# Performance work log

Hardware: AMD Instinct MI355X
Metric: run time of the kernel (lower is better)

The kernel has to match this reference:

```python
import jax, jax.numpy as jnp
import numpy as np
from jax import lax

RADIUS = 3
ITERATION = 6
KSIZE = 2 * RADIUS + 1


def _make_kernels(r):
    # Build the 8 directional side-window box kernels, order: L,R,U,D,NW,NE,SW,SE
    k = 2 * r + 1
    f = np.ones((k, k), np.float32)
    L = f.copy(); L[:, r + 1:] = 0
    R = f.copy(); R[:, :r] = 0
    U = f.copy(); U[r + 1:, :] = 0
    D = f.copy(); D[:r, :] = 0
    NW = U.copy(); NW[:, r + 1:] = 0
    NE = U.copy(); NE[:, :r] = 0
    SW = D.copy(); SW[:, r + 1:] = 0
    SE = D.copy(); SE[:, :r] = 0
    n_half = (r + 1) * k          # normalizer for half windows
    n_quarter = (r + 1) ** 2      # normalizer for quarter windows
    ks = np.stack([L / n_half, R / n_half, U / n_half, D / n_half,
                   NW / n_quarter, NE / n_quarter, SW / n_quarter, SE / n_quarter])
    return jnp.asarray(ks[:, None, :, :])  # (8,1,k,k) OIHW


def setup_inputs() -> dict:
    key = jax.random.key(0)
    k1, k2 = jax.random.split(key)
    im = jax.random.normal(k1, (4, 3, 512, 512), dtype=jnp.float32)
    pert = jax.random.normal(k2, (4, 3, 512, 512), dtype=jnp.float32)
    return {"im": im, "pert": pert}


def reference(im, pert):
    b, c, h, w = im.shape
    W = _make_kernels(RADIUS)

    def conv8(x):  # (N,1,h,w) -> (N,8,h,w), SAME padding of radius
        return lax.conv_general_dilated(
            x, W, window_strides=(1, 1),
            padding=[(RADIUS, RADIUS), (RADIUS, RADIUS)],
            dimension_numbers=("NCHW", "OIHW", "NCHW"))

    # channels are processed independently with identical kernels -> fold c into batch
    im_f = im.reshape(b * c, 1, h, w)
    pert_f = pert.reshape(b * c, 1, h, w)

    def step(carry, _):
        im_ch, pert_ch = carry
        z = jnp.concatenate([im_ch, pert_ch], axis=0)  # (2N,1,h,w)
        dz = conv8(z) - z                              # (2N,8,h,w), broadcast over dir
        d, dd = jnp.split(dz, 2, axis=0)
        idx = jnp.argmin(jnp.abs(d), axis=1, keepdims=True)    # (N,1,h,w)
        dm = jnp.take_along_axis(d, idx, axis=1)
        ddm = jnp.take_along_axis(dd, idx, axis=1)
        return (im_ch + dm, pert_ch + ddm), None

    (im_f, pert_f), _ = lax.scan(step, (im_f, pert_f), None, length=ITERATION)
    # torch code overwrites every channel of res with pert_ch -> result is filtered pert
    return pert_f.reshape(b, c, h, w)
```

## Files before the change

### kernel.cpp

```cpp
#include <hip/hip_runtime.h>

#define HH 512
#define WW 512
#define NIMG 12
#define RAD 3
#define TW 64
#define TH 16
#define LW (TW + 2*RAD)
#define LH (TH + 2*RAD)
#define RPW 4

typedef float v2 __attribute__((ext_vector_type(2)));

__global__ __launch_bounds__(256) void swf_step(
    const float* __restrict__ im_in, const float* __restrict__ pe_in,
    float* __restrict__ im_out, float* __restrict__ pe_out)
{
    __shared__ float sI[LH][LW];
    __shared__ float sP[LH][LW];

    const int tid = threadIdx.x;
    const int x0 = blockIdx.x * TW;
    const int y0 = blockIdx.y * TH;
    const size_t base = (size_t)blockIdx.z * (size_t)(HH * WW);
    const float* imb = im_in + base;
    const float* peb = pe_in + base;

    for (int i = tid; i < LH * LW; i += 256) {
        int r = i / LW;
        int c = i - r * LW;
        int gy = y0 - RAD + r;
        int gx = x0 - RAD + c;
        bool ok = ((unsigned)gy < (unsigned)HH) && ((unsigned)gx < (unsigned)WW);
        int gi = gy * WW + gx;
        sI[r][c] = ok ? imb[gi] : 0.0f;
        sP[r][c] = ok ? peb[gi] : 0.0f;
    }
    __syncthreads();

    const float w28 = 1.0f / 28.0f;
    const float w16 = 0.0625f;
    const v2 w28v = {w28, w28};
    const v2 w16v = {w16, w16};
    const int tx = tid & 63;
    const int wv = tid >> 6;
    const int r0 = wv * RPW;

    float wi[7][7];
    v2    hlr[7];
    float cc[7];

    #pragma unroll
    for (int m = 0; m < 7; ++m) {
        #pragma unroll
        for (int dx = 0; dx < 7; ++dx)
            wi[m][dx] = sI[r0 + m][tx + dx];
        float b0 = sP[r0 + m][tx],     b1 = sP[r0 + m][tx + 1],
              b2 = sP[r0 + m][tx + 2], b3 = sP[r0 + m][tx + 3],
              b4 = sP[r0 + m][tx + 4], b5 = sP[r0 + m][tx + 5],
              b6 = sP[r0 + m][tx + 6];
        hlr[m] = (v2){(b0 + b1) + (b2 + b3), (b3 + b4) + (b5 + b6)};
        cc[m] = b3;
    }

    #pragma unroll
    for (int jj = 0; jj < RPW; ++jj) {
        v2 aLR = {0.f, 0.f};
        v2 aUD = {0.f, 0.f};
        v2 aQN = {0.f, 0.f};
        v2 aQS = {0.f, 0.f};
        #pragma unroll
        for (int dy = 0; dy < 7; ++dy) {
            const int s = (jj + dy) % 7;
            #pragma unroll
            for (int dx = 0; dx < 4; ++dx)
                aLR = __builtin_elementwise_fma(
                    (v2){wi[s][dx], wi[s][dx + 3]}, w28v, aLR);
        }
        #pragma unroll
        for (int dy = 0; dy < 4; ++dy) {
            const int su = (jj + dy) % 7;
            const int sd = (jj + dy + 3) % 7;
            #pragma unroll
            for (int dx = 0; dx < 7; ++dx)
                aUD = __builtin_elementwise_fma(
                    (v2){wi[su][dx], wi[sd][dx]}, w28v, aUD);
            #pragma unroll
            for (int dx = 0; dx < 4; ++dx) {
                aQN = __builtin_elementwise_fma(
                    (v2){wi[su][dx], wi[su][dx + 3]}, w16v, aQN);
                aQS = __builtin_elementwise_fma(
                    (v2){wi[sd][dx], wi[sd][dx + 3]}, w16v, aQS);
            }
        }

        const float cI = wi[(jj + 3) % 7][3];
        const v2 cI2 = {cI, cI};
        const v2 d01 = aLR - cI2;
        const v2 d23 = aUD - cI2;
        const v2 d45 = aQN - cI2;
        const v2 d67 = aQS - cI2;
        float d[8] = {d01.x, d01.y, d23.x, d23.y, d45.x, d45.y, d67.x, d67.y};

        float e[8];
        const int p0 = (jj + 0) % 7, p1 = (jj + 1) % 7, p2 = (jj + 2) % 7,
                  p3 = (jj + 3) % 7, p4 = (jj + 4) % 7, p5 = (jj + 5) % 7,
                  p6 = (jj + 6) % 7;
        const float cP = cc[p3];
        {
            v2 qN = ((hlr[p0] + hlr[p1]) + (hlr[p2] + hlr[p3]));
            v2 qS = ((hlr[p3] + hlr[p4]) + (hlr[p5] + hlr[p6]));
            float cu = ((cc[p0] + cc[p1]) + (cc[p2] + cc[p3]));
            float cd = ((cc[p3] + cc[p4]) + (cc[p5] + cc[p6]));
            const v2 cP2 = {cP, cP};
            v2 eLR = (qN + qS - hlr[p3]) * w28v - cP2;
            v2 eQN = qN * w16v - cP2;
            v2 eQS = qS * w16v - cP2;
            e[0] = eLR.x;  e[1] = eLR.y;
            e[2] = (qN.x + qN.y - cu) * w28 - cP;
            e[3] = (qS.x + qS.y - cd) * w28 - cP;
            e[4] = eQN.x;  e[5] = eQN.y;
            e[6] = eQS.x;  e[7] = eQS.y;
        }

        float bestAbs = fabsf(d[0]);
        float bd = d[0];
        float be = e[0];
        #pragma unroll
        for (int j = 1; j < 8; ++j) {
            float a = fabsf(d[j]);
            bool take = a < bestAbs;
            bestAbs = take ? a : bestAbs;
            bd = take ? d[j] : bd;
            be = take ? e[j] : be;
        }

        const int gy = y0 + r0 + jj;
        const int gx = x0 + tx;
        const size_t gi = base + (size_t)gy * WW + gx;
        im_out[gi] = cI + bd;
        pe_out[gi] = cP + be;

        if (jj < RPW - 1) {
            const int m = r0 + jj + 7;
            const int slot = jj % 7;
            #pragma unroll
            for (int dx = 0; dx < 7; ++dx)
                wi[slot][dx] = sI[m][tx + dx];
            float b0 = sP[m][tx],     b1 = sP[m][tx + 1], b2 = sP[m][tx + 2],
                  b3 = sP[m][tx + 3], b4 = sP[m][tx + 4], b5 = sP[m][tx + 5],
                  b6 = sP[m][tx + 6];
            hlr[slot] = (v2){(b0 + b1) + (b2 + b3), (b3 + b4) + (b5 + b6)};
            cc[slot] = b3;
        }
    }
}

extern "C" void kernel_launch(void* const* d_in, const int* in_sizes, int n_in,
                              void* d_out, int out_size, void* d_ws, size_t ws_size,
                              hipStream_t stream) {
    const float* im0 = (const float*)d_in[0];
    const float* pe0 = (const float*)d_in[1];
    float* out = (float*)d_out;

    const size_t npix = (size_t)NIMG * HH * WW;
    float* imA = (float*)d_ws;
    float* imB = imA + npix;
    float* peA = imB + npix;
    float* peB = out;

    dim3 grid(WW / TW, HH / TH, NIMG);
    dim3 block(256);

    swf_step<<<grid, block, 0, stream>>>(im0, pe0, imA, peA);
    swf_step<<<grid, block, 0, stream>>>(imA, peA, imB, peB);
    swf_step<<<grid, block, 0, stream>>>(imB, peB, imA, peA);
    swf_step<<<grid, block, 0, stream>>>(imA, peA, imB, peB);
    swf_step<<<grid, block, 0, stream>>>(imB, peB, imA, peA);
    swf_step<<<grid, block, 0, stream>>>(imA, peA, imB, out);
}
```

Baseline: 235.9 us.

## Fuse two filter iterations per kernel via shared-memory halo recompute

Each launch now runs two side-window iterations: it loads a 12-pixel-halo tile, computes an intermediate 38x64 region into a second shared buffer (zeroing out-of-image pixels to mimic SAME padding), then computes the final 32x58 tile from it. This halves the number of launches and the global-memory round trips, at the cost of redundant halo computation and a narrower 58-column output tile. The intermediate image write is also skipped on the last launch, and the register window is stored as pre-paired vectors for packed FMAs.

```diff
diff --git a/kernel.cpp b/kernel.cpp
--- a/kernel.cpp
+++ b/kernel.cpp
@@ -4,103 +4,88 @@
 #define WW 512
 #define NIMG 12
 #define RAD 3
-#define TW 64
-#define TH 16
-#define LW (TW + 2*RAD)
-#define LH (TH + 2*RAD)
-#define RPW 4
+
+#define TW 58
+#define TH 32
+#define IW 64
+#define IH 38
+#define IW2 72
+#define SW 70
+#define SH 46
+#define GX ((WW + TW - 1) / TW)
 
 typedef float v2 __attribute__((ext_vector_type(2)));
 
-__global__ __launch_bounds__(256) void swf_step(
-    const float* __restrict__ im_in, const float* __restrict__ pe_in,
-    float* __restrict__ im_out, float* __restrict__ pe_out)
+template <int RPW, int LDW, class F>
+__device__ __forceinline__ void ring_pass(
+    const float* __restrict__ SI, const float* __restrict__ SP,
+    int r0, int tx, F emit)
 {
-    __shared__ float sI[LH][LW];
-    __shared__ float sP[LH][LW];
-
-    const int tid = threadIdx.x;
-    const int x0 = blockIdx.x * TW;
-    const int y0 = blockIdx.y * TH;
-    const size_t base = (size_t)blockIdx.z * (size_t)(HH * WW);
-    const float* imb = im_in + base;
-    const float* peb = pe_in + base;
-
-    for (int i = tid; i < LH * LW; i += 256) {
-        int r = i / LW;
-        int c = i - r * LW;
-        int gy = y0 - RAD + r;
-        int gx = x0 - RAD + c;
-        bool ok = ((unsigned)gy < (unsigned)HH) && ((unsigned)gx < (unsigned)WW);
-        int gi = gy * WW + gx;
-        sI[r][c] = ok ? imb[gi] : 0.0f;
-        sP[r][c] = ok ? peb[gi] : 0.0f;
-    }
-    __syncthreads();
-
     const float w28 = 1.0f / 28.0f;
     const float w16 = 0.0625f;
     const v2 w28v = {w28, w28};
     const v2 w16v = {w16, w16};
-    const int tx = tid & 63;
-    const int wv = tid >> 6;
-    const int r0 = wv * RPW;
-
-    float wi[7][7];
+
+    v2    pi[7][4];
     v2    hlr[7];
     float cc[7];
 
+    auto rowload = [&](int slot, int m) {
+        const float* rI = SI + m * LDW + tx;
+        float w0 = rI[0], w1 = rI[1], w2 = rI[2], w3 = rI[3],
+              w4 = rI[4], w5 = rI[5], w6 = rI[6];
+        pi[slot][0] = (v2){w0, w3};
+        pi[slot][1] = (v2){w1, w4};
+        pi[slot][2] = (v2){w2, w5};
+        pi[slot][3] = (v2){w3, w6};
+        const float* rP = SP + m * LDW + tx;
+        float b0 = rP[0], b1 = rP[1], b2 = rP[2], b3 = rP[3],
+              b4 = rP[4], b5 = rP[5], b6 = rP[6];
+        hlr[slot] = (v2){(b0 + b1) + (b2 + b3), (b3 + b4) + (b5 + b6)};
+        cc[slot] = b3;
+    };
+
     #pragma unroll
-    for (int m = 0; m < 7; ++m) {
-        #pragma unroll
-        for (int dx = 0; dx < 7; ++dx)
-            wi[m][dx] = sI[r0 + m][tx + dx];
-        float b0 = sP[r0 + m][tx],     b1 = sP[r0 + m][tx + 1],
-              b2 = sP[r0 + m][tx + 2], b3 = sP[r0 + m][tx + 3],
-              b4 = sP[r0 + m][tx + 4], b5 = sP[r0 + m][tx + 5],
-              b6 = sP[r0 + m][tx + 6];
-        hlr[m] = (v2){(b0 + b1) + (b2 + b3), (b3 + b4) + (b5 + b6)};
-        cc[m] = b3;
-    }
+    for (int m = 0; m < 7; ++m)
+        rowload(m, r0 + m);
 
     #pragma unroll
     for (int jj = 0; jj < RPW; ++jj) {
-        v2 aLR = {0.f, 0.f};
-        v2 aUD = {0.f, 0.f};
-        v2 aQN = {0.f, 0.f};
-        v2 aQS = {0.f, 0.f};
+        v2 aLR = {0.f, 0.f}, aQN = {0.f, 0.f}, aQS = {0.f, 0.f};
         #pragma unroll
         for (int dy = 0; dy < 7; ++dy) {
             const int s = (jj + dy) % 7;
             #pragma unroll
             for (int dx = 0; dx < 4; ++dx)
-                aLR = __builtin_elementwise_fma(
-                    (v2){wi[s][dx], wi[s][dx + 3]}, w28v, aLR);
-        }
+                aLR = __builtin_elementwise_fma(pi[s][dx], w28v, aLR);
+        }
+        float U = 0.f, Dd = 0.f;
         #pragma unroll
         for (int dy = 0; dy < 4; ++dy) {
             const int su = (jj + dy) % 7;
             const int sd = (jj + dy + 3) % 7;
-            #pragma unroll
-            for (int dx = 0; dx < 7; ++dx)
-                aUD = __builtin_elementwise_fma(
-                    (v2){wi[su][dx], wi[sd][dx]}, w28v, aUD);
+            U = fmaf(pi[su][0].x, w28, U);  U = fmaf(pi[su][1].x, w28, U);
+            U = fmaf(pi[su][2].x, w28, U);  U = fmaf(pi[su][3].x, w28, U);
+            U = fmaf(pi[su][1].y, w28, U);  U = fmaf(pi[su][2].y, w28, U);
+            U = fmaf(pi[su][3].y, w28, U);
+            Dd = fmaf(pi[sd][0].x, w28, Dd); Dd = fmaf(pi[sd][1].x, w28, Dd);
+            Dd = fmaf(pi[sd][2].x, w28, Dd); Dd = fmaf(pi[sd][3].x, w28, Dd);
+            Dd = fmaf(pi[sd][1].y, w28, Dd); Dd = fmaf(pi[sd][2].y, w28, Dd);
+            Dd = fmaf(pi[sd][3].y, w28, Dd);
             #pragma unroll
             for (int dx = 0; dx < 4; ++dx) {
-                aQN = __builtin_elementwise_fma(
-                    (v2){wi[su][dx], wi[su][dx + 3]}, w16v, aQN);
-                aQS = __builtin_elementwise_fma(
-                    (v2){wi[sd][dx], wi[sd][dx + 3]}, w16v, aQS);
+                aQN = __builtin_elementwise_fma(pi[su][dx], w16v, aQN);
+                aQS = __builtin_elementwise_fma(pi[sd][dx], w16v, aQS);
             }
         }
 
-        const float cI = wi[(jj + 3) % 7][3];
+        const float cI = pi[(jj + 3) % 7][3].x;
         const v2 cI2 = {cI, cI};
         const v2 d01 = aLR - cI2;
-        const v2 d23 = aUD - cI2;
+        const float d2 = U - cI, d3 = Dd - cI;
         const v2 d45 = aQN - cI2;
         const v2 d67 = aQS - cI2;
-        float d[8] = {d01.x, d01.y, d23.x, d23.y, d45.x, d45.y, d67.x, d67.y};
+        float d[8] = {d01.x, d01.y, d2, d3, d45.x, d45.y, d67.x, d67.y};
 
         float e[8];
         const int p0 = (jj + 0) % 7, p1 = (jj + 1) % 7, p2 = (jj + 2) % 7,
@@ -113,7 +98,7 @@
             float cu = ((cc[p0] + cc[p1]) + (cc[p2] + cc[p3]));
             float cd = ((cc[p3] + cc[p4]) + (cc[p5] + cc[p6]));
             const v2 cP2 = {cP, cP};
-            v2 eLR = (qN + qS - hlr[p3]) * w28v - cP2;
+            v2 eLR = (qN + qS - hlr[p3]) * (v2){1.0f/28.0f, 1.0f/28.0f} - cP2;
             v2 eQN = qN * w16v - cP2;
             v2 eQS = qS * w16v - cP2;
             e[0] = eLR.x;  e[1] = eLR.y;
@@ -135,24 +120,73 @@
             be = take ? e[j] : be;
         }
 
-        const int gy = y0 + r0 + jj;
-        const int gx = x0 + tx;
-        const size_t gi = base + (size_t)gy * WW + gx;
-        im_out[gi] = cI + bd;
-        pe_out[gi] = cP + be;
-
-        if (jj < RPW - 1) {
-            const int m = r0 + jj + 7;
-            const int slot = jj % 7;
-            #pragma unroll
-            for (int dx = 0; dx < 7; ++dx)
-                wi[slot][dx] = sI[m][tx + dx];
-            float b0 = sP[m][tx],     b1 = sP[m][tx + 1], b2 = sP[m][tx + 2],
-                  b3 = sP[m][tx + 3], b4 = sP[m][tx + 4], b5 = sP[m][tx + 5],
-                  b6 = sP[m][tx + 6];
-            hlr[slot] = (v2){(b0 + b1) + (b2 + b3), (b3 + b4) + (b5 + b6)};
-            cc[slot] = b3;
-        }
+        emit(jj, cI + bd, cP + be);
+
+        if (jj < RPW - 1)
+            rowload(jj % 7, r0 + jj + 7);
+    }
+}
+
+__global__ __launch_bounds__(256) void swf2(
+    const float* __restrict__ im_in, const float* __restrict__ pe_in,
+    float* __restrict__ im_out, float* __restrict__ pe_out, int storeIm)
+{
+    __shared__ float sI0[SH][SW];
+    __shared__ float sP0[SH][SW];
+    __shared__ float sI1[IH][IW2];
+    __shared__ float sP1[IH][IW2];
+
+    const int tid = threadIdx.x;
+    const int tx = tid & 63;
+    const int wv = tid >> 6;
+    const int x0 = blockIdx.x * TW;
+    const int y0 = blockIdx.y * TH;
+    const size_t ibase = (size_t)blockIdx.z * (size_t)(HH * WW);
+    const float* imb = im_in + ibase;
+    const float* peb = pe_in + ibase;
+
+    for (int i = tid; i < SH * SW; i += 256) {
+        int r = i / SW;
+        int c = i - r * SW;
+        int gy = y0 - 6 + r;
+        int gx = x0 - 6 + c;
+        bool ok = ((unsigned)gy < (unsigned)HH) && ((unsigned)gx < (unsigned)WW);
+        int gi = gy * WW + gx;
+        sI0[r][c] = ok ? imb[gi] : 0.0f;
+        sP0[r][c] = ok ? peb[gi] : 0.0f;
+    }
+    __syncthreads();
+
+    #pragma unroll 1
+    for (int pass = 0; pass < 2; ++pass) {
+        const int base = (wv + pass * 4) * 5;
+        ring_pass<5, SW>(&sI0[0][0], &sP0[0][0], base, tx,
+            [&](int jj, float vI, float vP) {
+                int ir = base + jj;
+                if (ir < IH) {
+                    int gy = y0 - 3 + ir;
+                    int gx = x0 - 3 + tx;
+                    bool ok = ((unsigned)gy < (unsigned)HH) &&
+                              ((unsigned)gx < (unsigned)WW);
+                    sI1[ir][tx] = ok ? vI : 0.0f;
+                    sP1[ir][tx] = ok ? vP : 0.0f;
+                }
+            });
+    }
+    __syncthreads();
+
+    #pragma unroll 1
+    for (int pass = 0; pass < 2; ++pass) {
+        const int base = (wv + pass * 4) * 4;
+        ring_pass<4, IW2>(&sI1[0][0], &sP1[0][0], base, tx,
+            [&](int jj, float vI, float vP) {
+                int gx = x0 + tx;
+                if (tx < TW && gx < WW) {
+                    size_t gi = ibase + (size_t)(y0 + base + jj) * WW + gx;
+                    if (storeIm) im_out[gi] = vI;
+                    pe_out[gi] = vP;
+                }
+            });
     }
 }
 
@@ -166,16 +200,12 @@
     const size_t npix = (size_t)NIMG * HH * WW;
     float* imA = (float*)d_ws;
     float* imB = imA + npix;
-    float* peA = imB + npix;
-    float* peB = out;
-
-    dim3 grid(WW / TW, HH / TH, NIMG);
+    float* peB = imB + npix;
+
+    dim3 grid(GX, HH / TH, NIMG);
     dim3 block(256);
 
-    swf_step<<<grid, block, 0, stream>>>(im0, pe0, imA, peA);
-    swf_step<<<grid, block, 0, stream>>>(imA, peA, imB, peB);
-    swf_step<<<grid, block, 0, stream>>>(imB, peB, imA, peA);
-    swf_step<<<grid, block, 0, stream>>>(imA, peA, imB, peB);
-    swf_step<<<grid, block, 0, stream>>>(imB, peB, imA, peA);
-    swf_step<<<grid, block, 0, stream>>>(imA, peA, imB, out);
+    swf2<<<grid, block, 0, stream>>>(im0, pe0, imA, out, 1);
+    swf2<<<grid, block, 0, stream>>>(imA, out, imB, peB, 1);
+    swf2<<<grid, block, 0, stream>>>(imB, peB, imA, out, 0);
 }
```

Result: slower. 255.9 us (+8.5%).
